# Kernel optimization log

Measured on AMD Instinct MI355X. Metric: run time of the kernel, lower is better.

## Reference

```python
import jax, jax.numpy as jnp
import numpy as np

B, D_IN, D_H = 16384, 512, 1024


def _glorot(key, out_d, in_d):
    lim = 1.0 / np.sqrt(in_d)
    return jax.random.uniform(key, (out_d, in_d), minval=-lim, maxval=lim, dtype=jnp.float32)


def setup_inputs() -> dict:
    key = jax.random.key(0)
    ks = jax.random.split(key, 16)
    inp = {
        "x_t": jax.random.normal(ks[0], (B, D_IN), dtype=jnp.float32),
        "delta_t": jax.random.uniform(ks[1], (B, 1), dtype=jnp.float32),
        "h_prev": jax.random.normal(ks[2], (B, D_H), dtype=jnp.float32),
        # torch nn.Linear weights are [out, in]; y = x @ W.T
        "W_sh": _glorot(ks[3], D_H, D_H),
        "W_sx": _glorot(ks[4], D_H, D_IN),
        "W_st": _glorot(ks[5], D_H, 1),
        "b_s": jnp.zeros((D_H,), jnp.float32),
        "WTh": _glorot(ks[6], D_H, D_H),
        "WTx": _glorot(ks[7], D_H, D_IN),
        "WTs": _glorot(ks[8], D_H, D_H),
        "b_T": jnp.zeros((D_H,), jnp.float32),
        "W_rh": _glorot(ks[9], D_H, D_H),
        "W_rx": _glorot(ks[10], D_H, D_IN),
        "b_r": jnp.zeros((D_H,), jnp.float32),
        "W_zh": _glorot(ks[11], D_H, D_H),
        "W_zx": _glorot(ks[12], D_H, D_IN),
        "b_z": jnp.zeros((D_H,), jnp.float32),
        "W_h": _glorot(ks[13], D_H, D_H),
        "W_x": _glorot(ks[14], D_H, D_IN),
        "b": jnp.zeros((D_H,), jnp.float32),
    }
    return inp


def reference(x_t, delta_t, h_prev,
              W_sh, W_sx, W_st, b_s,
              WTh, WTx, WTs, b_T,
              W_rh, W_rx, b_r,
              W_zh, W_zx, b_z,
              W_h, W_x, b):
    lin = lambda x, W: x @ W.T  # nn.Linear(bias=False)
    s_t = jnp.tanh(lin(h_prev, W_sh) + lin(x_t, W_sx) + lin(delta_t, W_st) + b_s)
    T_t = jax.nn.sigmoid(lin(h_prev, WTh) + lin(x_t, WTx) + lin(s_t, WTs) + b_T)
    r_t = jax.nn.sigmoid(lin(h_prev, W_rh) + lin(x_t, W_rx) + b_r)
    z_t = jax.nn.sigmoid(lin(h_prev, W_zh) + lin(x_t, W_zx) + b_z)
    h_tilde = jnp.tanh(lin(r_t * h_prev, W_h) + lin(x_t, W_x) + b)
    h_t = (1.0 - z_t) * (T_t * h_prev) + z_t * h_tilde
    return h_t
```

## Files before the change

kernel.cpp:

```cpp
#include <hip/hip_runtime.h>
#include <stdint.h>

#define AS1 __attribute__((address_space(1)))
#define AS3 __attribute__((address_space(3)))

typedef unsigned short US;
typedef __bf16 bf16x8 __attribute__((ext_vector_type(8)));
typedef float f32x4 __attribute__((ext_vector_type(4)));

static constexpr int Bsz = 16384;
static constexpr int DIN = 512;
static constexpr int DH  = 1024;
static constexpr int LDA = 1536;

__device__ __forceinline__ US f2bf(float f) {
  unsigned u = __float_as_uint(f);
  u += 0x7fffu + ((u >> 16) & 1u);
  return (US)(u >> 16);
}
__device__ __forceinline__ float bf2f(US u) { return __uint_as_float(((unsigned)u) << 16); }
__device__ __forceinline__ float sigm(float x) { return 1.f / (1.f + __expf(-x)); }
__device__ __forceinline__ float tanh_f(float x) { return 1.f - 2.f / (1.f + __expf(2.f * x)); }

__global__ void pack_A(const float* __restrict__ h, const float* __restrict__ x,
                       US* __restrict__ Ab) {
  const int total = Bsz * 384;
  for (int idx = blockIdx.x * blockDim.x + threadIdx.x; idx < total;
       idx += gridDim.x * blockDim.x) {
    int row = idx / 384;
    int c = (idx - row * 384) * 4;
    const float* src = (c < DH) ? (h + (size_t)row * DH + c)
                                : (x + (size_t)row * DIN + (c - DH));
    float4 v = *(const float4*)src;
    ushort4 o;
    o.x = f2bf(v.x); o.y = f2bf(v.y); o.z = f2bf(v.z); o.w = f2bf(v.w);
    *(ushort4*)(Ab + (size_t)row * LDA + c) = o;
  }
}

struct WSlot { const float* src; US* dst; int n4; };
struct WBatch { WSlot s[11]; };
__global__ void conv_w(WBatch b) {
  WSlot sl = b.s[blockIdx.y];
  for (int i = blockIdx.x * blockDim.x + threadIdx.x; i < sl.n4;
       i += gridDim.x * blockDim.x) {
    float4 v = *(const float4*)(sl.src + (size_t)i * 4);
    ushort4 o;
    o.x = f2bf(v.x); o.y = f2bf(v.y); o.z = f2bf(v.z); o.w = f2bf(v.w);
    *(ushort4*)(sl.dst + (size_t)i * 4) = o;
  }
}

template <int EPI, int KT0, int KT1, int KT2>
__global__ __launch_bounds__(256) void gemm_ep(
    const US* __restrict__ A0, int lda0,
    const US* __restrict__ A1, int lda1,
    const US* __restrict__ A2, int lda2,
    const US* __restrict__ W0, int ldw0,
    const US* __restrict__ W1, int ldw1,
    const US* __restrict__ W2, int ldw2,
    const float* __restrict__ bias,
    const void* aux0, const void* aux1, const void* aux2,
    void* outp, int ldo) {
  __shared__ __align__(16) US As[128 * 64];
  __shared__ __align__(16) US Bs[128 * 64];

  const int tid  = threadIdx.x;
  const int lane = tid & 63;
  const int w    = tid >> 6;

  const int p = blockIdx.x + (int)(gridDim.x * blockIdx.y);
  const int c = p & 7;
  const int q = p >> 3;
  const int nIdx = q & 7;
  const int mIdx = c * 16 + (q >> 3);
  const int mBase = mIdx * 128;
  const int nBase = nIdx * 128;

  f32x4 acc[4][4];
#pragma unroll
  for (int i = 0; i < 4; i++)
#pragma unroll
    for (int j = 0; j < 4; j++) acc[i][j] = f32x4{0.f, 0.f, 0.f, 0.f};

  const int rowL = w * 32 + (lane >> 3);
  const int cc   = lane & 7;
  const int scc  = cc ^ ((lane >> 3) & 7);
  const int gOff = scc * 8;
  const int wm = (w & 1) * 64, wn = (w >> 1) * 64;
  const int quad = lane >> 4, l15 = lane & 15;
  const int sw = l15 & 7;

#define K_TILE_LOOP(Ap, lda, Wp, ldw, KT)                                          \
  {                                                                                \
    const US* ga = (Ap) + (size_t)(mBase + rowL) * (lda) + gOff;                   \
    const US* gw = (Wp) + (size_t)(nBase + rowL) * (ldw) + gOff;                   \
    const size_t a8 = (size_t)8 * (lda), w8 = (size_t)8 * (ldw);                   \
    for (int k = 0; k < (KT); ++k) {                                               \
      _Pragma("unroll")                                                            \
      for (int i = 0; i < 4; i++) {                                                \
        __builtin_amdgcn_global_load_lds((AS1 const void*)(ga + i * a8),           \
            (AS3 void*)&As[(w * 32 + i * 8) * 64], 16, 0, 0);                      \
        __builtin_amdgcn_global_load_lds((AS1 const void*)(gw + i * w8),           \
            (AS3 void*)&Bs[(w * 32 + i * 8) * 64], 16, 0, 0);                      \
      }                                                                            \
      __builtin_amdgcn_s_waitcnt(0x0f70);                                          \
      __syncthreads();                                                             \
      _Pragma("unroll")                                                            \
      for (int ks = 0; ks < 2; ++ks) {                                             \
        bf16x8 af[4], bw[4];                                                       \
        _Pragma("unroll")                                                          \
        for (int i = 0; i < 4; i++)                                                \
          af[i] = *(const bf16x8*)&As[(wm + i * 16 + l15) * 64 +                   \
                                      (((ks * 4 + quad) ^ sw) * 8)];               \
        _Pragma("unroll")                                                          \
        for (int j = 0; j < 4; j++)                                                \
          bw[j] = *(const bf16x8*)&Bs[(wn + j * 16 + l15) * 64 +                   \
                                      (((ks * 4 + quad) ^ sw) * 8)];               \
        _Pragma("unroll")                                                          \
        for (int i = 0; i < 4; i++)                                                \
          _Pragma("unroll")                                                        \
          for (int j = 0; j < 4; j++)                                              \
            acc[i][j] = __builtin_amdgcn_mfma_f32_16x16x32_bf16(af[i], bw[j],      \
                                                                acc[i][j], 0, 0, 0);\
      }                                                                            \
      __syncthreads();                                                             \
      ga += 64; gw += 64;                                                          \
    }                                                                              \
  }

  if constexpr (KT0 > 0) K_TILE_LOOP(A0, lda0, W0, ldw0, KT0);
  if constexpr (KT1 > 0) K_TILE_LOOP(A1, lda1, W1, ldw1, KT1);
  if constexpr (KT2 > 0) K_TILE_LOOP(A2, lda2, W2, ldw2, KT2);
#undef K_TILE_LOOP

#pragma unroll
  for (int i = 0; i < 4; i++) {
#pragma unroll
    for (int j = 0; j < 4; j++) {
      const int col = nBase + wn + j * 16 + l15;
      const float bv = bias[col];
#pragma unroll
      for (int r = 0; r < 4; r++) {
        const int row = mBase + wm + i * 16 + quad * 4 + r;
        float v = acc[i][j][r] + bv;
        if constexpr (EPI == 0) {
          const float* delta = (const float*)aux0;
          const float* wst   = (const float*)aux1;
          v += delta[row] * wst[col];
          ((US*)outp)[(size_t)row * ldo + col] = f2bf(tanh_f(v));
        } else if constexpr (EPI == 1) {
          const float* hp = (const float*)aux0;
          float rr = sigm(v);
          ((US*)outp)[(size_t)row * ldo + col] =
              f2bf(rr * hp[(size_t)row * DH + col]);
        } else if constexpr (EPI == 2) {
          ((US*)outp)[(size_t)row * ldo + col] = f2bf(sigm(v));
        } else if constexpr (EPI == 3) {
          ((US*)outp)[(size_t)row * ldo + col] = f2bf(tanh_f(v));
        } else {
          const float* hp = (const float*)aux0;
          const US* Zp = (const US*)aux1;
          const US* Hp = (const US*)aux2;
          float T = sigm(v);
          size_t o = (size_t)row * DH + col;
          float z = bf2f(Zp[o]), ht = bf2f(Hp[o]);
          float h = hp[o];
          ((float*)outp)[(size_t)row * ldo + col] = (1.f - z) * (T * h) + z * ht;
        }
      }
    }
  }
}

extern "C" void kernel_launch(void* const* d_in, const int* in_sizes, int n_in,
                              void* d_out, int out_size, void* d_ws, size_t ws_size,
                              hipStream_t stream) {
  const float* x_t   = (const float*)d_in[0];
  const float* delta = (const float*)d_in[1];
  const float* h_prev= (const float*)d_in[2];
  const float* W_sh  = (const float*)d_in[3];
  const float* W_sx  = (const float*)d_in[4];
  const float* W_st  = (const float*)d_in[5];
  const float* b_s   = (const float*)d_in[6];
  const float* WTh   = (const float*)d_in[7];
  const float* WTx   = (const float*)d_in[8];
  const float* WTs   = (const float*)d_in[9];
  const float* b_T   = (const float*)d_in[10];
  const float* W_rh  = (const float*)d_in[11];
  const float* W_rx  = (const float*)d_in[12];
  const float* b_r   = (const float*)d_in[13];
  const float* W_zh  = (const float*)d_in[14];
  const float* W_zx  = (const float*)d_in[15];
  const float* b_z   = (const float*)d_in[16];
  const float* W_h   = (const float*)d_in[17];
  const float* W_x   = (const float*)d_in[18];
  const float* b_    = (const float*)d_in[19];
  float* out = (float*)d_out;

  char* ws = (char*)d_ws;
  US* Ab = (US*)ws;                         size_t off = (size_t)Bsz * LDA * 2;
  US* Sb = (US*)(ws + off);                 off += (size_t)Bsz * DH * 2;
  US* RH = (US*)(ws + off);                 off += (size_t)Bsz * DH * 2;
  US* Zb = (US*)(ws + off);                 off += (size_t)Bsz * DH * 2;
  US* HTb = (US*)(ws + off);                off += (size_t)Bsz * DH * 2;
  const size_t WHH = (size_t)DH * DH * 2, WHX = (size_t)DH * DIN * 2;
  US* bWsh = (US*)(ws + off); off += WHH;
  US* bWsx = (US*)(ws + off); off += WHX;
  US* bWTh = (US*)(ws + off); off += WHH;
  US* bWTx = (US*)(ws + off); off += WHX;
  US* bWTs = (US*)(ws + off); off += WHH;
  US* bWrh = (US*)(ws + off); off += WHH;
  US* bWrx = (US*)(ws + off); off += WHX;
  US* bWzh = (US*)(ws + off); off += WHH;
  US* bWzx = (US*)(ws + off); off += WHX;
  US* bWh  = (US*)(ws + off); off += WHH;
  US* bWx  = (US*)(ws + off); off += WHX;

  pack_A<<<dim3(8192), 256, 0, stream>>>(h_prev, x_t, Ab);
  WBatch wb;
  const int n4h = DH * DH / 4, n4x = DH * DIN / 4;
  wb.s[0]  = {W_sh, bWsh, n4h};  wb.s[1]  = {W_sx, bWsx, n4x};
  wb.s[2]  = {WTh,  bWTh, n4h};  wb.s[3]  = {WTx,  bWTx, n4x};
  wb.s[4]  = {WTs,  bWTs, n4h};  wb.s[5]  = {W_rh, bWrh, n4h};
  wb.s[6]  = {W_rx, bWrx, n4x};  wb.s[7]  = {W_zh, bWzh, n4h};
  wb.s[8]  = {W_zx, bWzx, n4x};  wb.s[9]  = {W_h,  bWh,  n4h};
  wb.s[10] = {W_x,  bWx,  n4x};
  conv_w<<<dim3(512, 11), 256, 0, stream>>>(wb);

  dim3 grid(DH / 128, Bsz / 128);
  const US* A_h = Ab;
  const US* A_x = Ab + DH;

  gemm_ep<0, 16, 8, 0><<<grid, 256, 0, stream>>>(
      A_h, LDA, A_x, LDA, nullptr, 0,
      bWsh, DH, bWsx, DIN, nullptr, 0,
      b_s, delta, W_st, nullptr, (void*)Sb, DH);
  gemm_ep<1, 16, 8, 0><<<grid, 256, 0, stream>>>(
      A_h, LDA, A_x, LDA, nullptr, 0,
      bWrh, DH, bWrx, DIN, nullptr, 0,
      b_r, h_prev, nullptr, nullptr, (void*)RH, DH);
  gemm_ep<2, 16, 8, 0><<<grid, 256, 0, stream>>>(
      A_h, LDA, A_x, LDA, nullptr, 0,
      bWzh, DH, bWzx, DIN, nullptr, 0,
      b_z, nullptr, nullptr, nullptr, (void*)Zb, DH);
  gemm_ep<3, 16, 8, 0><<<grid, 256, 0, stream>>>(
      RH, DH, A_x, LDA, nullptr, 0,
      bWh, DH, bWx, DIN, nullptr, 0,
      b_, nullptr, nullptr, nullptr, (void*)HTb, DH);
  gemm_ep<4, 16, 8, 16><<<grid, 256, 0, stream>>>(
      A_h, LDA, A_x, LDA, Sb, DH,
      bWTh, DH, bWTx, DIN, bWTs, DH,
      b_T, h_prev, Zb, HTb, (void*)out, DH);
}
```

Baseline: 655.8 us.

## Fuse s/r/z gate GEMMs into one wide GEMM with packed concatenated weights

Packs the h- and x-weights of each gate side by side into a single K=1536 bf16 matrix, so each gate is one contiguous K loop over the packed activations. The s, r and z gates become one GEMM with N=3072, and the epilogue picks the gate from the column block. The number of GEMM launches drops from five to three, and the shared A operand is read once for all three gates. The output tile shrinks to 128x64 with a launch-bounds occupancy hint to keep more blocks resident, at the cost of less data reuse per tile and a branchy epilogue.

```diff
diff --git a/kernel.cpp b/kernel.cpp
--- a/kernel.cpp
+++ b/kernel.cpp
@@ -12,6 +12,7 @@
 static constexpr int DIN = 512;
 static constexpr int DH  = 1024;
 static constexpr int LDA = 1536;
+static constexpr int LDW = 1536;
 
 __device__ __forceinline__ US f2bf(float f) {
   unsigned u = __float_as_uint(f);
@@ -38,32 +39,46 @@
   }
 }
 
-struct WSlot { const float* src; US* dst; int n4; };
-struct WBatch { WSlot s[11]; };
-__global__ void conv_w(WBatch b) {
-  WSlot sl = b.s[blockIdx.y];
-  for (int i = blockIdx.x * blockDim.x + threadIdx.x; i < sl.n4;
-       i += gridDim.x * blockDim.x) {
-    float4 v = *(const float4*)(sl.src + (size_t)i * 4);
+struct PairJob { const float* hW; const float* xW; US* dst; };
+struct PairBatch { PairJob j[5]; };
+__global__ void conv_pair(PairBatch b) {
+  PairJob jb = b.j[blockIdx.y];
+  const int total = DH * 384;
+  for (int idx = blockIdx.x * blockDim.x + threadIdx.x; idx < total;
+       idx += gridDim.x * blockDim.x) {
+    int r = idx / 384;
+    int c = (idx - r * 384) * 4;
+    const float* src = (c < DH) ? (jb.hW + (size_t)r * DH + c)
+                                : (jb.xW + (size_t)r * DIN + (c - DH));
+    float4 v = *(const float4*)src;
     ushort4 o;
     o.x = f2bf(v.x); o.y = f2bf(v.y); o.z = f2bf(v.z); o.w = f2bf(v.w);
-    *(ushort4*)(sl.dst + (size_t)i * 4) = o;
-  }
-}
-
-template <int EPI, int KT0, int KT1, int KT2>
-__global__ __launch_bounds__(256) void gemm_ep(
+    *(ushort4*)(jb.dst + (size_t)r * LDW + c) = o;
+  }
+}
+
+__global__ void conv_plain(const float* __restrict__ src, US* __restrict__ dst, int n4) {
+  for (int i = blockIdx.x * blockDim.x + threadIdx.x; i < n4;
+       i += gridDim.x * blockDim.x) {
+    float4 v = *(const float4*)(src + (size_t)i * 4);
+    ushort4 o;
+    o.x = f2bf(v.x); o.y = f2bf(v.y); o.z = f2bf(v.z); o.w = f2bf(v.w);
+    *(ushort4*)(dst + (size_t)i * 4) = o;
+  }
+}
+
+template <int EPI, int KT0, int KT1, int NX>
+__global__ __launch_bounds__(256, 6) void gemm_ep(
     const US* __restrict__ A0, int lda0,
     const US* __restrict__ A1, int lda1,
-    const US* __restrict__ A2, int lda2,
     const US* __restrict__ W0, int ldw0,
     const US* __restrict__ W1, int ldw1,
-    const US* __restrict__ W2, int ldw2,
-    const float* __restrict__ bias,
+    const float* __restrict__ b0, const float* __restrict__ b1,
+    const float* __restrict__ b2,
     const void* aux0, const void* aux1, const void* aux2,
-    void* outp, int ldo) {
+    void* out0, void* out1, void* out2) {
   __shared__ __align__(16) US As[128 * 64];
-  __shared__ __align__(16) US Bs[128 * 64];
+  __shared__ __align__(16) US Bs[64 * 64];
 
   const int tid  = threadIdx.x;
   const int lane = tid & 63;
@@ -72,55 +87,56 @@
   const int p = blockIdx.x + (int)(gridDim.x * blockIdx.y);
   const int c = p & 7;
   const int q = p >> 3;
-  const int nIdx = q & 7;
-  const int mIdx = c * 16 + (q >> 3);
+  const int nIdx = q % NX;
+  const int mIdx = c * 16 + q / NX;
   const int mBase = mIdx * 128;
-  const int nBase = nIdx * 128;
-
-  f32x4 acc[4][4];
+  const int nBase = nIdx * 64;
+
+  f32x4 acc[4][2];
 #pragma unroll
   for (int i = 0; i < 4; i++)
 #pragma unroll
-    for (int j = 0; j < 4; j++) acc[i][j] = f32x4{0.f, 0.f, 0.f, 0.f};
-
-  const int rowL = w * 32 + (lane >> 3);
-  const int cc   = lane & 7;
-  const int scc  = cc ^ ((lane >> 3) & 7);
+    for (int j = 0; j < 2; j++) acc[i][j] = f32x4{0.f, 0.f, 0.f, 0.f};
+
+  const int rowA = w * 32 + (lane >> 3);
+  const int rowB = w * 16 + (lane >> 3);
+  const int scc  = (lane & 7) ^ ((lane >> 3) & 7);
   const int gOff = scc * 8;
-  const int wm = (w & 1) * 64, wn = (w >> 1) * 64;
+  const int wm = (w & 1) * 64, wn = (w >> 1) * 32;
   const int quad = lane >> 4, l15 = lane & 15;
   const int sw = l15 & 7;
 
 #define K_TILE_LOOP(Ap, lda, Wp, ldw, KT)                                          \
   {                                                                                \
-    const US* ga = (Ap) + (size_t)(mBase + rowL) * (lda) + gOff;                   \
-    const US* gw = (Wp) + (size_t)(nBase + rowL) * (ldw) + gOff;                   \
+    const US* ga = (Ap) + (size_t)(mBase + rowA) * (lda) + gOff;                   \
+    const US* gw = (Wp) + (size_t)(nBase + rowB) * (ldw) + gOff;                   \
     const size_t a8 = (size_t)8 * (lda), w8 = (size_t)8 * (ldw);                   \
     for (int k = 0; k < (KT); ++k) {                                               \
       _Pragma("unroll")                                                            \
-      for (int i = 0; i < 4; i++) {                                                \
+      for (int i = 0; i < 4; i++)                                                  \
         __builtin_amdgcn_global_load_lds((AS1 const void*)(ga + i * a8),           \
             (AS3 void*)&As[(w * 32 + i * 8) * 64], 16, 0, 0);                      \
+      _Pragma("unroll")                                                            \
+      for (int i = 0; i < 2; i++)                                                  \
         __builtin_amdgcn_global_load_lds((AS1 const void*)(gw + i * w8),           \
-            (AS3 void*)&Bs[(w * 32 + i * 8) * 64], 16, 0, 0);                      \
-      }                                                                            \
+            (AS3 void*)&Bs[(w * 16 + i * 8) * 64], 16, 0, 0);                      \
       __builtin_amdgcn_s_waitcnt(0x0f70);                                          \
       __syncthreads();                                                             \
       _Pragma("unroll")                                                            \
       for (int ks = 0; ks < 2; ++ks) {                                             \
-        bf16x8 af[4], bw[4];                                                       \
+        bf16x8 af[4], bw[2];                                                       \
         _Pragma("unroll")                                                          \
         for (int i = 0; i < 4; i++)                                                \
           af[i] = *(const bf16x8*)&As[(wm + i * 16 + l15) * 64 +                   \
                                       (((ks * 4 + quad) ^ sw) * 8)];               \
         _Pragma("unroll")                                                          \
-        for (int j = 0; j < 4; j++)                                                \
+        for (int j = 0; j < 2; j++)                                                \
           bw[j] = *(const bf16x8*)&Bs[(wn + j * 16 + l15) * 64 +                   \
                                       (((ks * 4 + quad) ^ sw) * 8)];               \
         _Pragma("unroll")                                                          \
         for (int i = 0; i < 4; i++)                                                \
           _Pragma("unroll")                                                        \
-          for (int j = 0; j < 4; j++)                                              \
+          for (int j = 0; j < 2; j++)                                              \
             acc[i][j] = __builtin_amdgcn_mfma_f32_16x16x32_bf16(af[i], bw[j],      \
                                                                 acc[i][j], 0, 0, 0);\
       }                                                                            \
@@ -131,42 +147,48 @@
 
   if constexpr (KT0 > 0) K_TILE_LOOP(A0, lda0, W0, ldw0, KT0);
   if constexpr (KT1 > 0) K_TILE_LOOP(A1, lda1, W1, ldw1, KT1);
-  if constexpr (KT2 > 0) K_TILE_LOOP(A2, lda2, W2, ldw2, KT2);
 #undef K_TILE_LOOP
 
 #pragma unroll
   for (int i = 0; i < 4; i++) {
 #pragma unroll
-    for (int j = 0; j < 4; j++) {
+    for (int j = 0; j < 2; j++) {
       const int col = nBase + wn + j * 16 + l15;
-      const float bv = bias[col];
 #pragma unroll
       for (int r = 0; r < 4; r++) {
         const int row = mBase + wm + i * 16 + quad * 4 + r;
-        float v = acc[i][j][r] + bv;
+        float v = acc[i][j][r];
         if constexpr (EPI == 0) {
-          const float* delta = (const float*)aux0;
-          const float* wst   = (const float*)aux1;
-          v += delta[row] * wst[col];
-          ((US*)outp)[(size_t)row * ldo + col] = f2bf(tanh_f(v));
-        } else if constexpr (EPI == 1) {
-          const float* hp = (const float*)aux0;
-          float rr = sigm(v);
-          ((US*)outp)[(size_t)row * ldo + col] =
-              f2bf(rr * hp[(size_t)row * DH + col]);
-        } else if constexpr (EPI == 2) {
-          ((US*)outp)[(size_t)row * ldo + col] = f2bf(sigm(v));
+          const int gate = nBase >> 10;
+          const int cl = col & 1023;
+          if (gate == 0) {
+            const float* delta = (const float*)aux0;
+            const float* wst   = (const float*)aux1;
+            v += b0[cl] + delta[row] * wst[cl];
+            ((US*)out0)[(size_t)row * DH + cl] = f2bf(tanh_f(v));
+          } else if (gate == 1) {
+            const float* hp = (const float*)aux2;
+            v += b1[cl];
+            float rr = sigm(v);
+            ((US*)out1)[(size_t)row * DH + cl] =
+                f2bf(rr * hp[(size_t)row * DH + cl]);
+          } else {
+            v += b2[cl];
+            ((US*)out2)[(size_t)row * DH + cl] = f2bf(sigm(v));
+          }
         } else if constexpr (EPI == 3) {
-          ((US*)outp)[(size_t)row * ldo + col] = f2bf(tanh_f(v));
+          v += b0[col];
+          ((US*)out0)[(size_t)row * DH + col] = f2bf(tanh_f(v));
         } else {
           const float* hp = (const float*)aux0;
           const US* Zp = (const US*)aux1;
           const US* Hp = (const US*)aux2;
+          v += b0[col];
           float T = sigm(v);
           size_t o = (size_t)row * DH + col;
           float z = bf2f(Zp[o]), ht = bf2f(Hp[o]);
           float h = hp[o];
-          ((float*)outp)[(size_t)row * ldo + col] = (1.f - z) * (T * h) + z * ht;
+          ((float*)out0)[o] = (1.f - z) * (T * h) + z * ht;
         }
       }
     }
@@ -199,57 +221,47 @@
   float* out = (float*)d_out;
 
   char* ws = (char*)d_ws;
-  US* Ab = (US*)ws;                         size_t off = (size_t)Bsz * LDA * 2;
-  US* Sb = (US*)(ws + off);                 off += (size_t)Bsz * DH * 2;
-  US* RH = (US*)(ws + off);                 off += (size_t)Bsz * DH * 2;
-  US* Zb = (US*)(ws + off);                 off += (size_t)Bsz * DH * 2;
+  US* Ab  = (US*)ws;                        size_t off = (size_t)Bsz * LDA * 2;
+  US* Sb  = (US*)(ws + off);                off += (size_t)Bsz * DH * 2;
+  US* RH  = (US*)(ws + off);                off += (size_t)Bsz * DH * 2;
+  US* Zb  = (US*)(ws + off);                off += (size_t)Bsz * DH * 2;
   US* HTb = (US*)(ws + off);                off += (size_t)Bsz * DH * 2;
-  const size_t WHH = (size_t)DH * DH * 2, WHX = (size_t)DH * DIN * 2;
-  US* bWsh = (US*)(ws + off); off += WHH;
-  US* bWsx = (US*)(ws + off); off += WHX;
-  US* bWTh = (US*)(ws + off); off += WHH;
-  US* bWTx = (US*)(ws + off); off += WHX;
-  US* bWTs = (US*)(ws + off); off += WHH;
-  US* bWrh = (US*)(ws + off); off += WHH;
-  US* bWrx = (US*)(ws + off); off += WHX;
-  US* bWzh = (US*)(ws + off); off += WHH;
-  US* bWzx = (US*)(ws + off); off += WHX;
-  US* bWh  = (US*)(ws + off); off += WHH;
-  US* bWx  = (US*)(ws + off); off += WHX;
+  const size_t WPACK = (size_t)DH * LDW * 2;
+  US* bWsrz = (US*)(ws + off); off += 3 * WPACK;
+  US* bWhx  = (US*)(ws + off); off += WPACK;
+  US* bWThx = (US*)(ws + off); off += WPACK;
+  US* bWTs  = (US*)(ws + off); off += (size_t)DH * DH * 2;
 
   pack_A<<<dim3(8192), 256, 0, stream>>>(h_prev, x_t, Ab);
-  WBatch wb;
-  const int n4h = DH * DH / 4, n4x = DH * DIN / 4;
-  wb.s[0]  = {W_sh, bWsh, n4h};  wb.s[1]  = {W_sx, bWsx, n4x};
-  wb.s[2]  = {WTh,  bWTh, n4h};  wb.s[3]  = {WTx,  bWTx, n4x};
-  wb.s[4]  = {WTs,  bWTs, n4h};  wb.s[5]  = {W_rh, bWrh, n4h};
-  wb.s[6]  = {W_rx, bWrx, n4x};  wb.s[7]  = {W_zh, bWzh, n4h};
-  wb.s[8]  = {W_zx, bWzx, n4x};  wb.s[9]  = {W_h,  bWh,  n4h};
-  wb.s[10] = {W_x,  bWx,  n4x};
-  conv_w<<<dim3(512, 11), 256, 0, stream>>>(wb);
-
-  dim3 grid(DH / 128, Bsz / 128);
-  const US* A_h = Ab;
+  PairBatch pb;
+  pb.j[0] = {W_sh, W_sx, bWsrz};
+  pb.j[1] = {W_rh, W_rx, bWsrz + (size_t)DH * LDW};
+  pb.j[2] = {W_zh, W_zx, bWsrz + (size_t)2 * DH * LDW};
+  pb.j[3] = {W_h,  W_x,  bWhx};
+  pb.j[4] = {WTh,  WTx,  bWThx};
+  conv_pair<<<dim3(512, 5), 256, 0, stream>>>(pb);
+  conv_plain<<<dim3(512), 256, 0, stream>>>(WTs, bWTs, DH * DH / 4);
+
   const US* A_x = Ab + DH;
 
-  gemm_ep<0, 16, 8, 0><<<grid, 256, 0, stream>>>(
-      A_h, LDA, A_x, LDA, nullptr, 0,
-      bWsh, DH, bWsx, DIN, nullptr, 0,
-      b_s, delta, W_st, nullptr, (void*)Sb, DH);
-  gemm_ep<1, 16, 8, 0><<<grid, 256, 0, stream>>>(
-      A_h, LDA, A_x, LDA, nullptr, 0,
-      bWrh, DH, bWrx, DIN, nullptr, 0,
-      b_r, h_prev, nullptr, nullptr, (void*)RH, DH);
-  gemm_ep<2, 16, 8, 0><<<grid, 256, 0, stream>>>(
-      A_h, LDA, A_x, LDA, nullptr, 0,
-      bWzh, DH, bWzx, DIN, nullptr, 0,
-      b_z, nullptr, nullptr, nullptr, (void*)Zb, DH);
-  gemm_ep<3, 16, 8, 0><<<grid, 256, 0, stream>>>(
-      RH, DH, A_x, LDA, nullptr, 0,
-      bWh, DH, bWx, DIN, nullptr, 0,
-      b_, nullptr, nullptr, nullptr, (void*)HTb, DH);
-  gemm_ep<4, 16, 8, 16><<<grid, 256, 0, stream>>>(
-      A_h, LDA, A_x, LDA, Sb, DH,
-      bWTh, DH, bWTx, DIN, bWTs, DH,
-      b_T, h_prev, Zb, HTb, (void*)out, DH);
-}
+  gemm_ep<0, 24, 0, 48><<<dim3(48, 128), 256, 0, stream>>>(
+      Ab, LDA, nullptr, 0,
+      bWsrz, LDW, nullptr, 0,
+      b_s, b_r, b_z,
+      delta, W_st, h_prev,
+      (void*)Sb, (void*)RH, (void*)Zb);
+
+  gemm_ep<3, 16, 8, 16><<<dim3(16, 128), 256, 0, stream>>>(
+      RH, DH, A_x, LDA,
+      bWhx, LDW, bWhx + DH, LDW,
+      b_, nullptr, nullptr,
+      nullptr, nullptr, nullptr,
+      (void*)HTb, nullptr, nullptr);
+
+  gemm_ep<4, 24, 16, 16><<<dim3(16, 128), 256, 0, stream>>>(
+      Ab, LDA, Sb, DH,
+      bWThx, LDW, bWTs, DH,
+      b_T, nullptr, nullptr,
+      h_prev, Zb, HTb,
+      (void*)out, nullptr, nullptr);
+}
```

New measurement: 850.4 us. 1.3x slower.
